# Kernel tuning notes

Measured on AMD Instinct MI355X. Metric: run time of the kernel, lower is better.

## Reference

```python
import jax, jax.numpy as jnp
import numpy as np

B, C_H, C_L = 8, 128, 256
H_H, W_H = 64, 64
H_L, W_L = 128, 128
CS = 8
K = CS * CS  # 64 external keys (== inter_channels, matches hardcoded reatt dim)
EPS = 1e-5


def _bn(x, g, b, m, v):
    # inference-mode BatchNorm2d over channel dim 1
    scale = g / jnp.sqrt(v + EPS)
    return (x - m[None, :, None, None]) * scale[None, :, None, None] + b[None, :, None, None]


def setup_inputs() -> dict:
    key = jax.random.key(0)
    ks = jax.random.split(key, 13)
    return {
        "x_h": jax.random.normal(ks[0], (B, C_H, H_H, W_H), jnp.float32),
        "x_l": jax.random.normal(ks[1], (B, C_L, H_L, W_L), jnp.float32),
        "bn_h_gamma": jax.random.normal(ks[2], (C_H,), jnp.float32),
        "bn_h_beta": jax.random.normal(ks[3], (C_H,), jnp.float32),
        "bn_h_mean": jax.random.normal(ks[4], (C_H,), jnp.float32),
        "bn_h_var": jax.random.uniform(ks[5], (C_H,), jnp.float32),
        "kv_w": jax.random.normal(ks[6], (2 * C_L, C_H), jnp.float32) * 0.05,
        "kv_b": jax.random.normal(ks[7], (2 * C_L,), jnp.float32) * 0.05,
        "bn_l_gamma": jax.random.normal(ks[8], (C_L,), jnp.float32),
        "bn_l_beta": jax.random.normal(ks[9], (C_L,), jnp.float32),
        "bn_l_mean": jax.random.normal(ks[10], (C_L,), jnp.float32),
        "bn_l_var": jax.random.uniform(ks[11], (C_L,), jnp.float32),
        "reatt": jax.random.normal(ks[12], (1, K, 1, 1), jnp.float32) * 1e-5,
    }


def reference(x_h, x_l, bn_h_gamma, bn_h_beta, bn_h_mean, bn_h_var,
              kv_w, kv_b, bn_l_gamma, bn_l_beta, bn_l_mean, bn_l_var, reatt):
    # ---- cross_kv: BN -> AdaptiveMaxPool2d(8,8) -> 1x1 conv ----
    xh = _bn(x_h, bn_h_gamma, bn_h_beta, bn_h_mean, bn_h_var)
    # exact window max pool (H_H, W_H divisible by CS)
    p = xh.reshape(B, C_H, CS, H_H // CS, CS, W_H // CS).max(axis=(3, 5))  # [B,C_H,8,8]
    kv = jnp.einsum('bchw,oc->bohw', p, kv_w) + kv_b[None, :, None, None]  # [B,2*C_L,8,8]
    ck = kv[:, :C_L]   # [B,C_L,8,8]
    cv = kv[:, C_L:]   # [B,C_L,8,8]
    # cross_k: permute NHWC then flatten -> per-sample [K, C_L] key matrix
    ck = ck.transpose(0, 2, 3, 1).reshape(B, K, C_L)
    # cross_v: flatten spatial -> per-sample [C_L, K] value matrix
    cv = cv.reshape(B, C_L, K)

    # ---- ExternalAttention (use_cross_kv path) ----
    xl = _bn(x_l, bn_l_gamma, bn_l_beta, bn_l_mean, bn_l_var)
    # grouped 1x1 conv (groups=B) == per-sample projection onto K external keys
    attn = jnp.einsum('bchw,bkc->bkhw', xl, ck)          # [B,K,H_L,W_L]
    attn = attn + reatt                                   # broadcast [1,K,1,1]
    # _act_sn: scale by inter_channels^-0.5, softmax over the K key channels
    attn = jax.nn.softmax(attn * (K ** -0.5), axis=1)
    # grouped 1x1 conv with values: per-sample [C_L,K] @ [K,H*W]
    out = jnp.einsum('bkhw,bck->bchw', attn, cv)          # [B,C_L,H_L,W_L]
    return x_l + out
```

## Files before the change

### kernel.cpp

```cpp
#include <hip/hip_runtime.h>
#include <math.h>

#define B_     8
#define C_H_   128
#define C_L_   256
#define K_     64
#define NPIX_L 16384
#define EPS_   1e-5f

#define P_OFF     0
#define P_SZ      (B_*K_*C_H_)
#define B1_BYTE   (P_SZ*4)
#define B2_BYTE   (B1_BYTE + B_*K_*C_L_*2)
#define BIAS_BYTE (B2_BYTE + B_*K_*C_L_*2)

typedef short bf16x8 __attribute__((ext_vector_type(8)));
typedef float f32x4  __attribute__((ext_vector_type(4)));

__device__ inline unsigned short f2bf(float f) {
    unsigned int u = __float_as_uint(f);
    u += 0x7FFFu + ((u >> 16) & 1u);
    return (unsigned short)(u >> 16);
}
__device__ inline unsigned int pack2bf(float lo, float hi) {
    unsigned int ul = __float_as_uint(lo);
    unsigned int uh = __float_as_uint(hi);
    ul = (ul + (0x7FFFu + ((ul >> 16) & 1u))) >> 16;
    uh = (uh + (0x7FFFu + ((uh >> 16) & 1u))) & 0xFFFF0000u;
    return ul | uh;
}

#define MFMA16(a, b, c) __builtin_amdgcn_mfma_f32_16x16x32_bf16((a), (b), (c), 0, 0, 0)

#define GLOAD_LDS16(g, l) __builtin_amdgcn_global_load_lds( \
    (const __attribute__((address_space(1))) void*)(g), \
    (__attribute__((address_space(3))) void*)(l), 16, 0, 0)

__global__ __launch_bounds__(256) void pool_bn_kernel(
    const float* __restrict__ x_h,
    const float* __restrict__ g, const float* __restrict__ be,
    const float* __restrict__ mn, const float* __restrict__ vr,
    float* __restrict__ ws)
{
    const int t   = threadIdx.x;
    const int k   = t & 63;
    const int cl  = t >> 6;
    const int bid = blockIdx.x;
    const int b   = bid >> 5;
    const int c   = ((bid & 31) << 2) + cl;

    const float* plane = x_h + ((size_t)(b * C_H_ + c) << 12);
    const int ph = k >> 3, pw = k & 7;
    const float* p0 = plane + (ph * 8) * 64 + pw * 8;

    float mx = -INFINITY, mnv = INFINITY;
#pragma unroll
    for (int i = 0; i < 8; i++) {
        const float4 a  = *reinterpret_cast<const float4*>(p0 + i * 64);
        const float4 bq = *reinterpret_cast<const float4*>(p0 + i * 64 + 4);
        mx  = fmaxf(mx,  fmaxf(fmaxf(a.x, a.y),  fmaxf(a.z, a.w)));
        mx  = fmaxf(mx,  fmaxf(fmaxf(bq.x, bq.y), fmaxf(bq.z, bq.w)));
        mnv = fminf(mnv, fminf(fminf(a.x, a.y),  fminf(a.z, a.w)));
        mnv = fminf(mnv, fminf(fminf(bq.x, bq.y), fminf(bq.z, bq.w)));
    }
    const float sc  = g[c] * rsqrtf(vr[c] + EPS_);
    const float sel = (sc >= 0.f) ? mx : mnv;
    ws[P_OFF + (b * K_ + k) * C_H_ + c] = fmaf(sel - mn[c], sc, be[c]);
}

__global__ __launch_bounds__(256) void kv_kernel(
    const float* __restrict__ kv_w, const float* __restrict__ kv_b,
    const float* __restrict__ lg, const float* __restrict__ lb,
    const float* __restrict__ lm, const float* __restrict__ lv,
    const float* __restrict__ ratt,
    float* __restrict__ ws)
{
    __shared__ __align__(16) float plds[4 * 132];
    __shared__ float red[4][4];
    const int t    = threadIdx.x;
    const int lane = t & 63;
    const int wid  = t >> 6;
    const int bid  = blockIdx.x;
    const int b    = bid >> 5;
    const int kg   = (bid >> 1) & 15;
    const int oh   = bid & 1;

    if (t < 128) {
        const int px = t >> 5, u = t & 31;
        const float4 v = *reinterpret_cast<const float4*>(
            ws + P_OFF + (size_t)(b * K_ + kg * 4 + px) * C_H_ + u * 4);
        *reinterpret_cast<float4*>(plds + px * 132 + u * 4) = v;
    }
    __syncthreads();

    const int oi = t >> 2;
    const int q4 = t & 3;
    const int kk = kg * 4 + q4;

    unsigned short* b1 = (unsigned short*)((char*)ws + B1_BYTE);
    unsigned short* b2 = (unsigned short*)((char*)ws + B2_BYTE);

    float bc = 0.f;
#pragma unroll
    for (int pass = 0; pass < 4; pass++) {
        const int o = oh * 256 + pass * 64 + oi;
        const float* wrow = kv_w + (size_t)o * C_H_ + q4 * 4;
        float a0 = 0.f, a1 = 0.f, a2 = 0.f, a3 = 0.f;
#pragma unroll
        for (int i = 0; i < 8; i++) {
            const float4 wf = *reinterpret_cast<const float4*>(wrow + i * 16);
            const float4 p0 = *reinterpret_cast<const float4*>(plds + 0 * 132 + i * 16 + q4 * 4);
            const float4 p1 = *reinterpret_cast<const float4*>(plds + 1 * 132 + i * 16 + q4 * 4);
            const float4 p2 = *reinterpret_cast<const float4*>(plds + 2 * 132 + i * 16 + q4 * 4);
            const float4 p3 = *reinterpret_cast<const float4*>(plds + 3 * 132 + i * 16 + q4 * 4);
            a0 = fmaf(wf.x, p0.x, a0); a0 = fmaf(wf.y, p0.y, a0);
            a0 = fmaf(wf.z, p0.z, a0); a0 = fmaf(wf.w, p0.w, a0);
            a1 = fmaf(wf.x, p1.x, a1); a1 = fmaf(wf.y, p1.y, a1);
            a1 = fmaf(wf.z, p1.z, a1); a1 = fmaf(wf.w, p1.w, a1);
            a2 = fmaf(wf.x, p2.x, a2); a2 = fmaf(wf.y, p2.y, a2);
            a2 = fmaf(wf.z, p2.z, a2); a2 = fmaf(wf.w, p2.w, a2);
            a3 = fmaf(wf.x, p3.x, a3); a3 = fmaf(wf.y, p3.y, a3);
            a3 = fmaf(wf.z, p3.z, a3); a3 = fmaf(wf.w, p3.w, a3);
        }
        a0 += __shfl_xor(a0, 1, 64); a0 += __shfl_xor(a0, 2, 64);
        a1 += __shfl_xor(a1, 1, 64); a1 += __shfl_xor(a1, 2, 64);
        a2 += __shfl_xor(a2, 1, 64); a2 += __shfl_xor(a2, 2, 64);
        a3 += __shfl_xor(a3, 1, 64); a3 += __shfl_xor(a3, 2, 64);
        float val = (q4 == 0) ? a0 : (q4 == 1) ? a1 : (q4 == 2) ? a2 : a3;
        val += kv_b[o];

        if (oh == 0) {
            const float s = lg[o] * rsqrtf(lv[o] + EPS_);
            const float h = fmaf(-lm[o], s, lb[o]);
            bc = fmaf(h, val, bc);
            const int s1 = o >> 5, j = o & 7;
            const int l  = ((o >> 3) & 3) * 16 + (kk & 15);
            const int n  = kk >> 4;
            b1[((((b * 8 + s1) * 4 + n) * 64) + l) * 8 + j] = f2bf(val * s);
        } else {
            const int co = o - 256;
            const int s2 = kk >> 5, j2 = kk & 7;
            const int l2 = ((kk >> 3) & 3) * 16 + (co & 15);
            const int n2 = co >> 4;
            b2[((((b * 2 + s2) * 16 + n2) * 64) + l2) * 8 + j2] = f2bf(val);
        }
    }

    if (oh == 0) {
#pragma unroll
        for (int m = 4; m < 64; m <<= 1) bc += __shfl_xor(bc, m, 64);
        if (lane < 4) red[wid][lane] = bc;
        __syncthreads();
        if (t < 4) {
            const float sum = red[0][t] + red[1][t] + red[2][t] + red[3][t];
            const int kkf = kg * 4 + t;
            float* bia = (float*)((char*)ws + BIAS_BYTE);
            bia[b * K_ + kkf] = (sum + ratt[kkf]) * 0.125f;
        }
    }
}

__global__ __launch_bounds__(256, 6) void attn_mfma(
    const float* __restrict__ x_l,
    const float* __restrict__ ws_f,
    float* __restrict__ out)
{
    __shared__ __align__(16) char lds[17920];
    float* xbuf0 = (float*)lds;
    float* xbuf1 = (float*)(lds + 8192);
    float* obuf  = (float*)lds;
    unsigned short* wscr = (unsigned short*)(lds + 8704);

    const int t    = threadIdx.x;
    const int lane = t & 63;
    const int wid  = t >> 6;
    const int bid  = blockIdx.x;
    const int b    = bid & 7;
    const int tile = bid >> 3;
    const int px0  = tile * 64;
    const int r16  = lane & 15;
    const int q    = lane >> 4;

    const unsigned short* b1 = (const unsigned short*)((const char*)ws_f + B1_BYTE);
    const unsigned short* b2 = (const unsigned short*)((const char*)ws_f + B2_BYTE);
    const float* biasf = (const float*)((const char*)ws_f + BIAS_BYTE) + b * K_;
    const float* xb = x_l + (size_t)b * (C_L_ * NPIX_L);
    float* ob = out + (size_t)b * (C_L_ * NPIX_L);

    float bl[4];
#pragma unroll
    for (int n = 0; n < 4; n++) bl[n] = biasf[16 * n + r16];

    const int sd = lane >> 4;
    const int su = ((lane & 15) << 2) ^ ((wid & 1) << 4);
#define STAGE(bufp, s_) do { \
    _Pragma("unroll") \
    for (int i_ = 0; i_ < 2; i_++) { \
        const int cl_ = 8 * wid + 4 * i_; \
        const float* gp_ = xb + (size_t)(32 * (s_) + cl_ + sd) * NPIX_L + px0 + su; \
        GLOAD_LDS16(gp_, (bufp) + (size_t)cl_ * 64); \
    } \
} while (0)

    f32x4 acc1[4] = {};
    union ABu { bf16x8 v; unsigned int u[4]; };
    bf16x8 bfr[2][4];
    const bf16x8* bbase = ((const bf16x8*)b1) + (b * 8 * 4) * 64 + lane;

    STAGE(xbuf0, 0);
#pragma unroll
    for (int n = 0; n < 4; n++) bfr[0][n] = bbase[n * 64];

    const int p0x = (wid * 16 + r16) ^ ((q & 1) << 4);

#pragma unroll
    for (int s = 0; s < 8; s++) {
        const int p = s & 1;
        float* xbf = p ? xbuf1 : xbuf0;
        if (s < 7) {
            STAGE(p ? xbuf0 : xbuf1, s + 1);
            asm volatile("s_waitcnt vmcnt(2)" ::: "memory");
        } else {
            asm volatile("s_waitcnt vmcnt(0)" ::: "memory");
        }
        __builtin_amdgcn_s_barrier();

        if (s < 7) {
#pragma unroll
            for (int n = 0; n < 4; n++) bfr[p ^ 1][n] = bbase[((s + 1) * 4 + n) * 64];
        }

        ABu a0f;
#pragma unroll
        for (int jj = 0; jj < 4; jj++) {
            const float* row0 = xbf + (8 * q + 2 * jj) * 64;
            a0f.u[jj] = pack2bf(row0[p0x], row0[64 + p0x]);
        }
#pragma unroll
        for (int n = 0; n < 4; n++) acc1[n] = MFMA16(a0f.v, bfr[p][n], acc1[n]);
        __builtin_amdgcn_s_barrier();
    }

    unsigned short* wsb = wscr + wid * 1152;
#pragma unroll
    for (int r = 0; r < 4; r++) {
        float e0 = fmaf(acc1[0][r], 0.125f, bl[0]);
        float e1 = fmaf(acc1[1][r], 0.125f, bl[1]);
        float e2 = fmaf(acc1[2][r], 0.125f, bl[2]);
        float e3 = fmaf(acc1[3][r], 0.125f, bl[3]);
        float mx = fmaxf(fmaxf(e0, e1), fmaxf(e2, e3));
#pragma unroll
        for (int msk = 1; msk < 16; msk <<= 1) mx = fmaxf(mx, __shfl_xor(mx, msk, 64));
        e0 = __expf(e0 - mx); e1 = __expf(e1 - mx);
        e2 = __expf(e2 - mx); e3 = __expf(e3 - mx);
        float sm = (e0 + e1) + (e2 + e3);
#pragma unroll
        for (int msk = 1; msk < 16; msk <<= 1) sm += __shfl_xor(sm, msk, 64);
        const float inv = 1.f / sm;
        unsigned short* wp = wsb + (q * 4 + r) * 72 + r16;
        wp[0]  = f2bf(e0 * inv);
        wp[16] = f2bf(e1 * inv);
        wp[32] = f2bf(e2 * inv);
        wp[48] = f2bf(e3 * inv);
    }

    bf16x8 af[2];
#pragma unroll
    for (int s2 = 0; s2 < 2; s2++)
        af[s2] = *(const bf16x8*)(wsb + r16 * 72 + 32 * s2 + q * 8);

#pragma unroll
    for (int nc = 0; nc < 8; nc++) {
        f32x4 acc2[2] = {};
#pragma unroll
        for (int s2 = 0; s2 < 2; s2++) {
            const bf16x8* bp2 = ((const bf16x8*)b2) + ((b * 2 + s2) * 16 + nc * 2) * 64 + lane;
#pragma unroll
            for (int nn = 0; nn < 2; nn++) {
                const bf16x8 bfr2 = bp2[nn * 64];
                acc2[nn] = MFMA16(af[s2], bfr2, acc2[nn]);
            }
        }
#pragma unroll
        for (int nn = 0; nn < 2; nn++) {
            float* dp = obuf + (16 * nn + r16) * 68 + wid * 16 + 4 * q;
            *(f32x4*)dp = acc2[nn];
        }
        asm volatile("s_waitcnt lgkmcnt(0)" ::: "memory");
        __builtin_amdgcn_s_barrier();
        const int cbase = nc * 32;
#pragma unroll
        for (int u2 = 0; u2 < 2; u2++) {
            const int idx = t + 256 * u2;
            const int col = idx >> 4;
            const int un  = idx & 15;
            const float4 vv = *(const float4*)(obuf + col * 68 + un * 4);
            const size_t gbase = (size_t)(cbase + col) * NPIX_L + px0 + un * 4;
            const float4 xv4 = *(const float4*)(xb + gbase);
            float4 o;
            o.x = vv.x + xv4.x; o.y = vv.y + xv4.y;
            o.z = vv.z + xv4.z; o.w = vv.w + xv4.w;
            *(float4*)(ob + gbase) = o;
        }
        __builtin_amdgcn_s_barrier();
    }
#undef STAGE
}

extern "C" void kernel_launch(void* const* d_in, const int* in_sizes, int n_in,
                              void* d_out, int out_size, void* d_ws, size_t ws_size,
                              hipStream_t stream) {
    const float* x_h  = (const float*)d_in[0];
    const float* x_l  = (const float*)d_in[1];
    const float* hg   = (const float*)d_in[2];
    const float* hb   = (const float*)d_in[3];
    const float* hm   = (const float*)d_in[4];
    const float* hv   = (const float*)d_in[5];
    const float* kvw  = (const float*)d_in[6];
    const float* kvb  = (const float*)d_in[7];
    const float* lg   = (const float*)d_in[8];
    const float* lb   = (const float*)d_in[9];
    const float* lm   = (const float*)d_in[10];
    const float* lv   = (const float*)d_in[11];
    const float* ratt = (const float*)d_in[12];
    float* ws  = (float*)d_ws;
    float* out = (float*)d_out;

    pool_bn_kernel<<<256, 256, 0, stream>>>(x_h, hg, hb, hm, hv, ws);
    kv_kernel<<<256, 256, 0, stream>>>(kvw, kvb, lg, lb, lm, lv, ratt, ws);
    attn_mfma<<<2048, 256, 0, stream>>>(x_l, ws, out);
}
```

Before: 308.6 us.

## Enlarge attention pixel tile to 256 per block and prefetch residual

Each attention block now processes 256 pixels instead of 64. Each wave handles four 16-pixel M-tiles, which reuses the per-batch key and value B-fragments across four MFMAs and cuts the grid to 512 blocks. The residual x_l loads for the output stage are software-prefetched into registers one channel chunk ahead. LDS grows to about 70KB and launch bounds drop to 2 blocks per CU, so latency hiding and occupancy go down while register pressure goes up.

```diff
diff --git a/kernel.cpp b/kernel.cpp
--- a/kernel.cpp
+++ b/kernel.cpp
@@ -160,16 +160,16 @@
     }
 }
 
-__global__ __launch_bounds__(256, 6) void attn_mfma(
+__global__ __launch_bounds__(256, 2) void attn_mfma(
     const float* __restrict__ x_l,
     const float* __restrict__ ws_f,
     float* __restrict__ out)
 {
-    __shared__ __align__(16) char lds[17920];
+    __shared__ __align__(16) char lds[70144];
     float* xbuf0 = (float*)lds;
-    float* xbuf1 = (float*)(lds + 8192);
-    float* obuf  = (float*)lds;
-    unsigned short* wscr = (unsigned short*)(lds + 8704);
+    float* xbuf1 = (float*)(lds + 32768);
+    unsigned short* wscr = (unsigned short*)lds;
+    float* obuf = (float*)(lds + 36864);
 
     const int t    = threadIdx.x;
     const int lane = t & 63;
@@ -177,7 +177,7 @@
     const int bid  = blockIdx.x;
     const int b    = bid & 7;
     const int tile = bid >> 3;
-    const int px0  = tile * 64;
+    const int px0  = tile * 256;
     const int r16  = lane & 15;
     const int q    = lane >> 4;
 
@@ -191,18 +191,17 @@
 #pragma unroll
     for (int n = 0; n < 4; n++) bl[n] = biasf[16 * n + r16];
 
-    const int sd = lane >> 4;
-    const int su = ((lane & 15) << 2) ^ ((wid & 1) << 4);
+    const int sof = (lane << 2) ^ (wid << 4);
 #define STAGE(bufp, s_) do { \
     _Pragma("unroll") \
-    for (int i_ = 0; i_ < 2; i_++) { \
-        const int cl_ = 8 * wid + 4 * i_; \
-        const float* gp_ = xb + (size_t)(32 * (s_) + cl_ + sd) * NPIX_L + px0 + su; \
-        GLOAD_LDS16(gp_, (bufp) + (size_t)cl_ * 64); \
+    for (int i_ = 0; i_ < 8; i_++) { \
+        const int cl_ = 8 * wid + i_; \
+        const float* gp_ = xb + (size_t)(32 * (s_) + cl_) * NPIX_L + px0 + sof; \
+        GLOAD_LDS16(gp_, (bufp) + (size_t)cl_ * 256); \
     } \
 } while (0)
 
-    f32x4 acc1[4] = {};
+    f32x4 acc1[4][4] = {};
     union ABu { bf16x8 v; unsigned int u[4]; };
     bf16x8 bfr[2][4];
     const bf16x8* bbase = ((const bf16x8*)b1) + (b * 8 * 4) * 64 + lane;
@@ -211,15 +210,13 @@
 #pragma unroll
     for (int n = 0; n < 4; n++) bfr[0][n] = bbase[n * 64];
 
-    const int p0x = (wid * 16 + r16) ^ ((q & 1) << 4);
-
 #pragma unroll
     for (int s = 0; s < 8; s++) {
         const int p = s & 1;
-        float* xbf = p ? xbuf1 : xbuf0;
+        const float* xbf = p ? xbuf1 : xbuf0;
         if (s < 7) {
             STAGE(p ? xbuf0 : xbuf1, s + 1);
-            asm volatile("s_waitcnt vmcnt(2)" ::: "memory");
+            asm volatile("s_waitcnt vmcnt(8)" ::: "memory");
         } else {
             asm volatile("s_waitcnt vmcnt(0)" ::: "memory");
         }
@@ -230,76 +227,101 @@
             for (int n = 0; n < 4; n++) bfr[p ^ 1][n] = bbase[((s + 1) * 4 + n) * 64];
         }
 
-        ABu a0f;
-#pragma unroll
-        for (int jj = 0; jj < 4; jj++) {
-            const float* row0 = xbf + (8 * q + 2 * jj) * 64;
-            a0f.u[jj] = pack2bf(row0[p0x], row0[64 + p0x]);
-        }
-#pragma unroll
-        for (int n = 0; n < 4; n++) acc1[n] = MFMA16(a0f.v, bfr[p][n], acc1[n]);
+#pragma unroll
+        for (int m = 0; m < 4; m++) {
+            const int colm = (64 * wid + 16 * m + r16) ^ (q << 4);
+            ABu amf;
+#pragma unroll
+            for (int jj = 0; jj < 4; jj++) {
+                amf.u[jj] = pack2bf(xbf[(8 * q + 2 * jj) * 256 + colm],
+                                    xbf[(8 * q + 2 * jj + 1) * 256 + colm]);
+            }
+#pragma unroll
+            for (int n = 0; n < 4; n++)
+                acc1[m][n] = MFMA16(amf.v, bfr[p][n], acc1[m][n]);
+        }
         __builtin_amdgcn_s_barrier();
     }
 
-    unsigned short* wsb = wscr + wid * 1152;
-#pragma unroll
-    for (int r = 0; r < 4; r++) {
-        float e0 = fmaf(acc1[0][r], 0.125f, bl[0]);
-        float e1 = fmaf(acc1[1][r], 0.125f, bl[1]);
-        float e2 = fmaf(acc1[2][r], 0.125f, bl[2]);
-        float e3 = fmaf(acc1[3][r], 0.125f, bl[3]);
-        float mx = fmaxf(fmaxf(e0, e1), fmaxf(e2, e3));
-#pragma unroll
-        for (int msk = 1; msk < 16; msk <<= 1) mx = fmaxf(mx, __shfl_xor(mx, msk, 64));
-        e0 = __expf(e0 - mx); e1 = __expf(e1 - mx);
-        e2 = __expf(e2 - mx); e3 = __expf(e3 - mx);
-        float sm = (e0 + e1) + (e2 + e3);
-#pragma unroll
-        for (int msk = 1; msk < 16; msk <<= 1) sm += __shfl_xor(sm, msk, 64);
-        const float inv = 1.f / sm;
-        unsigned short* wp = wsb + (q * 4 + r) * 72 + r16;
-        wp[0]  = f2bf(e0 * inv);
-        wp[16] = f2bf(e1 * inv);
-        wp[32] = f2bf(e2 * inv);
-        wp[48] = f2bf(e3 * inv);
-    }
-
-    bf16x8 af[2];
-#pragma unroll
-    for (int s2 = 0; s2 < 2; s2++)
-        af[s2] = *(const bf16x8*)(wsb + r16 * 72 + 32 * s2 + q * 8);
-
+    unsigned short* wsb = wscr + wid * (64 * 72);
+#pragma unroll
+    for (int m = 0; m < 4; m++) {
+#pragma unroll
+        for (int r = 0; r < 4; r++) {
+            float e0 = fmaf(acc1[m][0][r], 0.125f, bl[0]);
+            float e1 = fmaf(acc1[m][1][r], 0.125f, bl[1]);
+            float e2 = fmaf(acc1[m][2][r], 0.125f, bl[2]);
+            float e3 = fmaf(acc1[m][3][r], 0.125f, bl[3]);
+            float mx = fmaxf(fmaxf(e0, e1), fmaxf(e2, e3));
+#pragma unroll
+            for (int msk = 1; msk < 16; msk <<= 1) mx = fmaxf(mx, __shfl_xor(mx, msk, 64));
+            e0 = __expf(e0 - mx); e1 = __expf(e1 - mx);
+            e2 = __expf(e2 - mx); e3 = __expf(e3 - mx);
+            float sm = (e0 + e1) + (e2 + e3);
+#pragma unroll
+            for (int msk = 1; msk < 16; msk <<= 1) sm += __shfl_xor(sm, msk, 64);
+            const float inv = 1.f / sm;
+            unsigned short* wp = wsb + (16 * m + q * 4 + r) * 72 + r16;
+            wp[0]  = f2bf(e0 * inv);
+            wp[16] = f2bf(e1 * inv);
+            wp[32] = f2bf(e2 * inv);
+            wp[48] = f2bf(e3 * inv);
+        }
+    }
+
+    bf16x8 af[4][2];
+#pragma unroll
+    for (int m = 0; m < 4; m++)
+#pragma unroll
+        for (int s2 = 0; s2 < 2; s2++)
+            af[m][s2] = *(const bf16x8*)(wsb + (16 * m + r16) * 72 + 32 * s2 + 8 * q);
+
+    float4 rv[2][8];
+#pragma unroll
+    for (int u2 = 0; u2 < 8; u2++) {
+        const int col = wid + 4 * u2;
+        rv[0][u2] = *(const float4*)(xb + (size_t)col * NPIX_L + px0 + lane * 4);
+    }
 #pragma unroll
     for (int nc = 0; nc < 8; nc++) {
-        f32x4 acc2[2] = {};
+        f32x4 acc2[4][2] = {};
 #pragma unroll
         for (int s2 = 0; s2 < 2; s2++) {
             const bf16x8* bp2 = ((const bf16x8*)b2) + ((b * 2 + s2) * 16 + nc * 2) * 64 + lane;
 #pragma unroll
             for (int nn = 0; nn < 2; nn++) {
-                const bf16x8 bfr2 = bp2[nn * 64];
-                acc2[nn] = MFMA16(af[s2], bfr2, acc2[nn]);
+                const bf16x8 b2f = bp2[nn * 64];
+#pragma unroll
+                for (int m = 0; m < 4; m++)
+                    acc2[m][nn] = MFMA16(af[m][s2], b2f, acc2[m][nn]);
             }
         }
 #pragma unroll
-        for (int nn = 0; nn < 2; nn++) {
-            float* dp = obuf + (16 * nn + r16) * 68 + wid * 16 + 4 * q;
-            *(f32x4*)dp = acc2[nn];
+        for (int m = 0; m < 4; m++)
+#pragma unroll
+            for (int nn = 0; nn < 2; nn++) {
+                float* dp = obuf + (16 * nn + r16) * 260 + 64 * wid + 16 * m + 4 * q;
+                *(f32x4*)dp = acc2[m][nn];
+            }
+        if (nc < 7) {
+#pragma unroll
+            for (int u2 = 0; u2 < 8; u2++) {
+                const int col = wid + 4 * u2;
+                rv[(nc + 1) & 1][u2] = *(const float4*)(
+                    xb + (size_t)((nc + 1) * 32 + col) * NPIX_L + px0 + lane * 4);
+            }
         }
         asm volatile("s_waitcnt lgkmcnt(0)" ::: "memory");
         __builtin_amdgcn_s_barrier();
-        const int cbase = nc * 32;
-#pragma unroll
-        for (int u2 = 0; u2 < 2; u2++) {
-            const int idx = t + 256 * u2;
-            const int col = idx >> 4;
-            const int un  = idx & 15;
-            const float4 vv = *(const float4*)(obuf + col * 68 + un * 4);
-            const size_t gbase = (size_t)(cbase + col) * NPIX_L + px0 + un * 4;
-            const float4 xv4 = *(const float4*)(xb + gbase);
+#pragma unroll
+        for (int u2 = 0; u2 < 8; u2++) {
+            const int col = wid + 4 * u2;
+            const float4 vv = *(const float4*)(obuf + col * 260 + lane * 4);
+            const float4 xr = rv[nc & 1][u2];
+            const size_t gbase = (size_t)(nc * 32 + col) * NPIX_L + px0 + lane * 4;
             float4 o;
-            o.x = vv.x + xv4.x; o.y = vv.y + xv4.y;
-            o.z = vv.z + xv4.z; o.w = vv.w + xv4.w;
+            o.x = vv.x + xr.x; o.y = vv.y + xr.y;
+            o.z = vv.z + xr.z; o.w = vv.w + xr.w;
             *(float4*)(ob + gbase) = o;
         }
         __builtin_amdgcn_s_barrier();
@@ -328,5 +350,5 @@
 
     pool_bn_kernel<<<256, 256, 0, stream>>>(x_h, hg, hb, hm, hv, ws);
     kv_kernel<<<256, 256, 0, stream>>>(kvw, kvb, lg, lb, lm, lv, ratt, ws);
-    attn_mfma<<<2048, 256, 0, stream>>>(x_l, ws, out);
-}
+    attn_mfma<<<512, 256, 0, stream>>>(x_l, ws, out);
+}
```

Result: faster. 294.3 us (-4.6%).
